# Optimization experiments

Hardware: AMD Instinct MI355X
Metric: run time of the kernel (lower is better)

## Reference

```python
import jax, jax.numpy as jnp
import numpy as np

DT = 0.01  # hard-coded timestep in _tt_floquet_forward_tf
OMEGA = 1.0  # drive_frequency default


def setup_inputs() -> dict:
    key = jax.random.key(0)
    k1, k2, k3, k4 = jax.random.split(key, 4)
    B, S, D, M = 4, 4096, 4096, 16
    x = jax.random.normal(k1, (B, S, D), dtype=jnp.float32)
    floquet_energies = jax.random.normal(k2, (M, D), dtype=jnp.float32) * 0.01  # RandomNormal(stddev=0.01)
    drive_weights = jax.random.normal(k3, (M,), dtype=jnp.float32)
    coupling_matrix = jax.random.normal(k4, (M, M), dtype=jnp.float32)
    return {
        "x": x,
        "floquet_energies": floquet_energies,
        "drive_weights": drive_weights,
        "coupling_matrix": coupling_matrix,
    }


def reference(x, floquet_energies, drive_weights, coupling_matrix):
    # Per the TF fallback, per timestep t:
    #   z_n = x_t * exp(-i n w t)                      (demodulate into Floquet modes)
    #   z_n <- z_n * exp(-i eps_n dt)                  (quasi-energy rotation)
    #   y_t = Re( sum_n z_n * exp(+i n w (t+dt)) )     (remodulate at t+dt)
    # The n*w*t phase cancels, leaving a time-independent per-dim gain:
    #   y[t,d] = x[t,d] * sum_n cos(n*w*dt - eps[n,d]*dt)
    # with eps[n,d] = floquet_energies[n,d] * (1 + 0.1 * drive_weights[n]).
    # coupling_matrix is unused by the fallback forward.
    modes = floquet_energies.shape[0]
    n = jnp.arange(modes, dtype=x.dtype)                                  # [M]
    eps = floquet_energies * (1.0 + 0.1 * drive_weights)[:, None]         # [M, D]
    coef = jnp.cos(n[:, None] * (OMEGA * DT) - eps * DT)                  # [M, D]
    gain = jnp.sum(coef, axis=0)                                          # [D]
    return x * gain  # [B, S, D]
```

## Files before the change

kernel.cpp:

```cpp
#include <hip/hip_runtime.h>


#define F_DT 0.01f
#define F_OMEGA 1.0f

__global__ void gain_kernel(const float* __restrict__ fe,
                            const float* __restrict__ dw,
                            float* __restrict__ gain, int M, int D) {
    int d = blockIdx.x * blockDim.x + threadIdx.x;
    if (d >= D) return;
    float g = 0.0f;
    for (int n = 0; n < M; ++n) {
        float eps = fe[(long long)n * D + d] * (1.0f + 0.1f * dw[n]);
        g += cosf((float)n * (F_OMEGA * F_DT) - eps * F_DT);
    }
    gain[d] = g;
}

__global__ void scale_kernel(const float4* __restrict__ x,
                             const float4* __restrict__ gain4,
                             float4* __restrict__ out,
                             long long n4, int Dq) {
    long long i = (long long)blockIdx.x * blockDim.x + threadIdx.x;
    if (i >= n4) return;
    long long di = ((Dq & (Dq - 1)) == 0) ? (i & (long long)(Dq - 1)) : (i % Dq);
    float4 xv = x[i];
    float4 gv = gain4[di];
    float4 o;
    o.x = xv.x * gv.x;
    o.y = xv.y * gv.y;
    o.z = xv.z * gv.z;
    o.w = xv.w * gv.w;
    out[i] = o;
}

extern "C" void kernel_launch(void* const* d_in, const int* in_sizes, int n_in,
                              void* d_out, int out_size, void* d_ws, size_t ws_size,
                              hipStream_t stream) {
    const float* x  = (const float*)d_in[0];
    const float* fe = (const float*)d_in[1];
    const float* dw = (const float*)d_in[2];

    float* out  = (float*)d_out;
    float* gain = (float*)d_ws;

    int M = in_sizes[2];
    int D = in_sizes[1] / M;
    long long n = (long long)in_sizes[0];

    {
        int threads = 256;
        int blocks = (D + threads - 1) / threads;
        gain_kernel<<<blocks, threads, 0, stream>>>(fe, dw, gain, M, D);
    }

    {
        long long n4 = n / 4;
        int Dq = D / 4;
        int threads = 256;
        long long blocks = (n4 + threads - 1) / threads;
        scale_kernel<<<(int)blocks, threads, 0, stream>>>(
            (const float4*)x, (const float4*)gain, (float4*)out, n4, Dq);
    }
}
```

Before: 430.3 us.

## Fuse gain computation into row-persistent scaling kernel with nontemporal streaming

Merges the gain and scale kernels into one launch. Each block has one thread per float4 column, recomputes the per-dimension gain in registers, and then walks a grid-strided set of rows scaling x with nontemporal loads and stores. This removes the second launch, the workspace round trip and the per-element gain gather. In exchange every block redundantly computes all the cosines for the row width (2048 blocks × 16 modes × 4096 dims), which is small next to the 256MB stream. A scalar fallback covers shapes where the row width does not fit the block layout.

```diff
diff --git a/kernel.cpp b/kernel.cpp
--- a/kernel.cpp
+++ b/kernel.cpp
@@ -4,34 +4,53 @@
 #define F_DT 0.01f
 #define F_OMEGA 1.0f
 
-__global__ void gain_kernel(const float* __restrict__ fe,
-                            const float* __restrict__ dw,
-                            float* __restrict__ gain, int M, int D) {
-    int d = blockIdx.x * blockDim.x + threadIdx.x;
-    if (d >= D) return;
-    float g = 0.0f;
+typedef float f32x4 __attribute__((ext_vector_type(4)));
+
+__global__ __launch_bounds__(1024) void fused_rows_kernel(
+        const f32x4* __restrict__ x4,
+        const f32x4* __restrict__ fe4,
+        const float* __restrict__ dw,
+        f32x4* __restrict__ out4,
+        int M, int Dq, long long n4) {
+    const int t = threadIdx.x;
+
+    f32x4 g = {0.0f, 0.0f, 0.0f, 0.0f};
+    #pragma unroll 4
     for (int n = 0; n < M; ++n) {
-        float eps = fe[(long long)n * D + d] * (1.0f + 0.1f * dw[n]);
-        g += cosf((float)n * (F_OMEGA * F_DT) - eps * F_DT);
+        f32x4 e = fe4[(long long)n * Dq + t];
+        float w = (1.0f + 0.1f * dw[n]) * F_DT;
+        float a = (float)n * (F_OMEGA * F_DT);
+        g.x += cosf(a - e.x * w);
+        g.y += cosf(a - e.y * w);
+        g.z += cosf(a - e.z * w);
+        g.w += cosf(a - e.w * w);
     }
-    gain[d] = g;
+
+    const long long stride = (long long)gridDim.x * Dq;
+    for (long long i = (long long)blockIdx.x * Dq + t; i < n4; i += stride) {
+        f32x4 xv = __builtin_nontemporal_load(&x4[i]);
+        f32x4 o = xv * g;
+        __builtin_nontemporal_store(o, &out4[i]);
+    }
 }
 
-__global__ void scale_kernel(const float4* __restrict__ x,
-                             const float4* __restrict__ gain4,
-                             float4* __restrict__ out,
-                             long long n4, int Dq) {
-    long long i = (long long)blockIdx.x * blockDim.x + threadIdx.x;
-    if (i >= n4) return;
-    long long di = ((Dq & (Dq - 1)) == 0) ? (i & (long long)(Dq - 1)) : (i % Dq);
-    float4 xv = x[i];
-    float4 gv = gain4[di];
-    float4 o;
-    o.x = xv.x * gv.x;
-    o.y = xv.y * gv.y;
-    o.z = xv.z * gv.z;
-    o.w = xv.w * gv.w;
-    out[i] = o;
+__global__ void fused_scalar_kernel(
+        const float* __restrict__ x,
+        const float* __restrict__ fe,
+        const float* __restrict__ dw,
+        float* __restrict__ out,
+        int M, int D, long long n) {
+    const long long stride = (long long)gridDim.x * blockDim.x;
+    for (long long i = (long long)blockIdx.x * blockDim.x + threadIdx.x;
+         i < n; i += stride) {
+        int d = (int)(i % D);
+        float g = 0.0f;
+        for (int nn = 0; nn < M; ++nn) {
+            float eps = fe[(long long)nn * D + d] * (1.0f + 0.1f * dw[nn]);
+            g += cosf((float)nn * (F_OMEGA * F_DT) - eps * F_DT);
+        }
+        out[i] = x[i] * g;
+    }
 }
 
 extern "C" void kernel_launch(void* const* d_in, const int* in_sizes, int n_in,
@@ -41,25 +60,28 @@
     const float* fe = (const float*)d_in[1];
     const float* dw = (const float*)d_in[2];
 
-    float* out  = (float*)d_out;
-    float* gain = (float*)d_ws;
+    float* out = (float*)d_out;
+    (void)d_ws; (void)ws_size;
 
     int M = in_sizes[2];
     int D = in_sizes[1] / M;
     long long n = (long long)in_sizes[0];
 
-    {
+    const int Dq = D / 4;
+    const bool vec_ok = (D % 4 == 0) && (n % D == 0) &&
+                        (Dq >= 64) && (Dq <= 1024) && (Dq % 64 == 0);
+
+    if (vec_ok) {
+        long long n4 = n / 4;
+        long long rows = n4 / Dq;
+        int blocks = (int)(rows < 2048 ? rows : 2048);
+        fused_rows_kernel<<<blocks, Dq, 0, stream>>>(
+            (const f32x4*)x, (const f32x4*)fe, dw, (f32x4*)out, M, Dq, n4);
+    } else {
         int threads = 256;
-        int blocks = (D + threads - 1) / threads;
-        gain_kernel<<<blocks, threads, 0, stream>>>(fe, dw, gain, M, D);
-    }
-
-    {
-        long long n4 = n / 4;
-        int Dq = D / 4;
-        int threads = 256;
-        long long blocks = (n4 + threads - 1) / threads;
-        scale_kernel<<<(int)blocks, threads, 0, stream>>>(
-            (const float4*)x, (const float4*)gain, (float4*)out, n4, Dq);
+        long long want = (n + threads - 1) / threads;
+        int blocks = (int)(want < 2048 ? want : 2048);
+        fused_scalar_kernel<<<blocks, threads, 0, stream>>>(
+            x, fe, dw, out, M, D, n);
     }
 }
```

Result: slower. 484.2 us (+12.5%).
